# Kernel optimization log

Hardware: AMD Instinct MI355X
Metric: run time of the kernel (lower is better)

The kernel has to match this reference:

```python
import jax, jax.numpy as jnp
import numpy as np

N, E, G = 10000, 40000, 64   # nodes, edges, graphs
ED, H, OUT = 4, 64, 4        # edge_attr_dim, hidden, output_dim


def _nnconv(x, src, dst, edge_attr, w1, b1, w2, b2, root_w, bias, in_dim, out_dim, n_nodes):
    # edge MLP: Linear -> ReLU -> Linear, producing per-edge [in_dim, out_dim] weights
    h = jax.nn.relu(edge_attr @ w1 + b1) @ w2 + b2        # [E, in*out]
    W = h.reshape(-1, in_dim, out_dim)                    # [E, in, out]
    msg = jnp.einsum('ei,eio->eo', x[src], W)             # gather + per-edge matmul
    s = jax.ops.segment_sum(msg, dst, num_segments=n_nodes)
    cnt = jax.ops.segment_sum(jnp.ones((msg.shape[0],), x.dtype), dst, num_segments=n_nodes)
    agg = s / jnp.maximum(cnt, 1.0)[:, None]              # scatter-mean (0 for isolated nodes)
    return agg + x @ root_w + bias                        # NNConv root weight + bias


def setup_inputs():
    key = jax.random.key(0)
    ks = jax.random.split(key, 16)
    lin = lambda k, i, o: jax.random.normal(k, (i, o), jnp.float32) * 0.05
    inp = {}
    inp['node_ids'] = jax.random.normal(ks[0], (N, 1), jnp.float32)
    inp['edge_index'] = jax.random.randint(ks[1], (2, E), 0, N)
    inp['edge_attr'] = jax.random.normal(ks[2], (E, ED), jnp.float32)
    inp['batch'] = jnp.sort(jax.random.randint(ks[3], (N,), 0, G))
    # layer 0: in=1, out=H
    inp['w1_0'] = lin(ks[4], ED, 1 * H); inp['b1_0'] = jnp.zeros((1 * H,), jnp.float32)
    inp['w2_0'] = lin(ks[5], 1 * H, 1 * H); inp['b2_0'] = jnp.zeros((1 * H,), jnp.float32)
    inp['root_0'] = lin(ks[6], 1, H); inp['bias_0'] = jnp.zeros((H,), jnp.float32)
    # layer 1: in=H, out=H
    inp['w1_1'] = lin(ks[7], ED, H * H); inp['b1_1'] = jnp.zeros((H * H,), jnp.float32)
    inp['w2_1'] = lin(ks[8], H * H, H * H); inp['b2_1'] = jnp.zeros((H * H,), jnp.float32)
    inp['root_1'] = lin(ks[9], H, H); inp['bias_1'] = jnp.zeros((H,), jnp.float32)
    # classifier
    inp['wc1'] = lin(ks[10], H, H); inp['bc1'] = jnp.zeros((H,), jnp.float32)
    inp['wc2'] = lin(ks[11], H, OUT); inp['bc2'] = jnp.zeros((OUT,), jnp.float32)
    return inp


def reference(node_ids, edge_index, edge_attr, batch,
              w1_0, b1_0, w2_0, b2_0, root_0, bias_0,
              w1_1, b1_1, w2_1, b2_1, root_1, bias_1,
              wc1, bc1, wc2, bc2):
    src, dst = edge_index[0], edge_index[1]
    x = node_ids
    x = jax.nn.relu(_nnconv(x, src, dst, edge_attr, w1_0, b1_0, w2_0, b2_0, root_0, bias_0, 1, H, N))
    x = jax.nn.relu(_nnconv(x, src, dst, edge_attr, w1_1, b1_1, w2_1, b2_1, root_1, bias_1, H, H, N))
    # dropout omitted (inference mode)
    gs = jax.ops.segment_sum(x, batch, num_segments=G)
    gc = jax.ops.segment_sum(jnp.ones((N,), x.dtype), batch, num_segments=G)
    pooled = gs / jnp.maximum(gc, 1.0)[:, None]           # global_mean_pool
    h = jax.nn.relu(pooled @ wc1 + bc1)
    return h @ wc2 + bc2
```

## Files before the change

kernel.cpp:

```cpp
#include <hip/hip_runtime.h>
#include <hip/hip_fp16.h>

#define N_NODES 10000
#define N_EDGES 40000
#define N_GRAPH 64
#define KKREAL  262144
#define KKTOT   262272
#define BROW    KKTOT
#define EPAD    40192
#define PSLICE  (EPAD * 64)

typedef _Float16 half8_t  __attribute__((ext_vector_type(8)));
typedef float    floatx16 __attribute__((ext_vector_type(16)));

__device__ __forceinline__ void gload_lds16(const void* g, void* l) {
  __builtin_amdgcn_global_load_lds((const __attribute__((address_space(1))) void*)g,
                                   (__attribute__((address_space(3))) void*)l, 16, 0, 0);
}

__device__ __host__ __forceinline__ int swz(int row) {
  return ((row & 3) << 1) | ((row >> 2) & 1);
}

__device__ __forceinline__ half8_t splat8(_Float16 v) {
  half8_t r = {v, v, v, v, v, v, v, v};
  return r;
}

__global__ void prep_B(const float* __restrict__ w2, const float* __restrict__ b2,
                       _Float16* __restrict__ Bws) {
  int kk = blockIdx.x * blockDim.x + threadIdx.x;
  if (kk >= KKTOT) return;
  int s = (kk >> 3) & 15, j3 = kk & 7;
  int basekk = kk & ~127;
  for (int o = 0; o < 64; ++o) {
    int kk_l = basekk | ((s ^ swz(o)) << 3) | j3;
    int k = kk_l >> 6, i = kk_l & 63;
    float v;
    if (k < 4096)       v = w2[k * 4096 + i * 64 + o];
    else if (k == 4096) v = b2[i * 64 + o];
    else                v = 0.f;
    Bws[(size_t)o * BROW + kk] = (_Float16)v;
  }
}

__global__ void layer0_edge(const float* __restrict__ node_ids,
                            const int* __restrict__ ei,
                            const float* __restrict__ ea,
                            const float* __restrict__ w1, const float* __restrict__ b1,
                            const float* __restrict__ w2, const float* __restrict__ b2,
                            float* __restrict__ agg0, float* __restrict__ cnt) {
  __shared__ float w1s[256], b1s[64], w2s[4096], b2s[64], zb[4][64];
  int t = threadIdx.x;
  for (int idx = t; idx < 4096; idx += 256) w2s[idx] = w2[idx];
  if (t < 256) w1s[t] = w1[t];
  if (t < 64) { b1s[t] = b1[t]; b2s[t] = b2[t]; }
  __syncthreads();
  int w = t >> 6, l = t & 63;
  int gw = blockIdx.x * 4 + w;
  int nw = gridDim.x * 4;
  for (int e = gw; e < N_EDGES; e += nw) {
    float a0 = ea[e * 4 + 0], a1 = ea[e * 4 + 1], a2 = ea[e * 4 + 2], a3 = ea[e * 4 + 3];
    float z = a0 * w1s[l] + a1 * w1s[64 + l] + a2 * w1s[128 + l] + a3 * w1s[192 + l] + b1s[l];
    zb[w][l] = fmaxf(z, 0.f);
    asm volatile("s_waitcnt lgkmcnt(0)" ::: "memory");
    __builtin_amdgcn_sched_barrier(0);
    float h = b2s[l];
    #pragma unroll
    for (int k = 0; k < 64; ++k) h += zb[w][k] * w2s[k * 64 + l];
    int src = ei[e], dst = ei[N_EDGES + e];
    float msg = node_ids[src] * h;
    atomicAdd(&agg0[dst * 64 + l], msg);
    if (l == 0) atomicAdd(&cnt[dst], 1.0f);
  }
}

__global__ void node0(const float* __restrict__ node_ids, const int* __restrict__ batch,
                      const float* __restrict__ agg0, const float* __restrict__ cnt,
                      const float* __restrict__ root0, const float* __restrict__ bias0,
                      float* __restrict__ x1, float* __restrict__ pcnt) {
  int gid = blockIdx.x * 256 + threadIdx.x;
  if (gid >= N_NODES * 64) return;
  int n = gid >> 6, o = gid & 63;
  float c = fmaxf(cnt[n], 1.f);
  float v = agg0[gid] / c + node_ids[n] * root0[o] + bias0[o];
  x1[gid] = fmaxf(v, 0.f);
  if (o == 0) atomicAdd(&pcnt[batch[n]], 1.0f);
}

template <bool PART>
__launch_bounds__(256, 3)
__global__ void fused_edge_gemm(const int* __restrict__ ei,
                                const float* __restrict__ ea,
                                const float* __restrict__ x1,
                                const float* __restrict__ w1, const float* __restrict__ b1,
                                const _Float16* __restrict__ Bws,
                                float* __restrict__ outbuf) {
  __shared__ __attribute__((aligned(16))) _Float16 Bl[2][64 * 128];
  __shared__ __attribute__((aligned(16))) __half2 w1q[256][4];
  __shared__ __half2 b1p[256];
  int t = threadIdx.x;
  int ks = blockIdx.x & 7;
  int eb = blockIdx.x >> 3;
  int e0 = eb * 256;
  int w = t >> 6, l = t & 63;
  int half_ = l >> 5;
  int lane31 = l & 31;
  int swo = swz(lane31);

  int kb = ks * 512;
  {
    int j = t;
    #pragma unroll
    for (int d = 0; d < 4; ++d) {
      float2 v = *(const float2*)(w1 + d * 4096 + kb + 2 * j);
      w1q[j][d] = __floats2half2_rn(v.x, v.y);
    }
    float2 bv = *(const float2*)(b1 + kb + 2 * j);
    b1p[j] = __floats2half2_rn(bv.x, bv.y);
  }

  half8_t xh8[2][4];
  __half2 eb_bc[2][4];
  #pragma unroll
  for (int m = 0; m < 2; ++m) {
    int e = e0 + w * 64 + m * 32 + lane31;
    if (e < N_EDGES) {
      int src = ei[e];
      const float* xp = x1 + src * 64 + half_ * 8;
      #pragma unroll
      for (int q = 0; q < 4; ++q) {
        float4 f0 = *(const float4*)(xp + q * 16);
        float4 f1 = *(const float4*)(xp + q * 16 + 4);
        half8_t v;
        v[0] = (_Float16)f0.x; v[1] = (_Float16)f0.y;
        v[2] = (_Float16)f0.z; v[3] = (_Float16)f0.w;
        v[4] = (_Float16)f1.x; v[5] = (_Float16)f1.y;
        v[6] = (_Float16)f1.z; v[7] = (_Float16)f1.w;
        xh8[m][q] = v;
      }
      float4 av = *(const float4*)(ea + e * 4);
      eb_bc[m][0] = __float2half2_rn(av.x); eb_bc[m][1] = __float2half2_rn(av.y);
      eb_bc[m][2] = __float2half2_rn(av.z); eb_bc[m][3] = __float2half2_rn(av.w);
    } else {
      #pragma unroll
      for (int q = 0; q < 4; ++q) xh8[m][q] = splat8((_Float16)0.f);
      #pragma unroll
      for (int d = 0; d < 4; ++d) eb_bc[m][d] = __float2half2_rn(0.f);
    }
  }

  floatx16 acc[2][2];
  #pragma unroll
  for (int m = 0; m < 2; ++m)
    #pragma unroll
    for (int n = 0; n < 2; ++n)
      #pragma unroll
      for (int r = 0; r < 16; ++r) acc[m][n][r] = 0.f;

  int nchunk = (ks == 7) ? 257 : 256;
  size_t sbase_b = (size_t)ks * 65536;
  const char* Bb = (const char*)Bws;

  const char* srcp[4];
  {
    int colb = (l & 15) * 16;
    #pragma unroll
    for (int j = 0; j < 4; ++j) {
      int row = w * 16 + j * 4 + (l >> 4);
      srcp[j] = Bb + sbase_b + (size_t)row * (BROW * 2) + colb;
    }
  }
  char* dst0 = (char*)&Bl[0][0] + w * 4096 + l * 16;
  char* dst1 = (char*)&Bl[1][0] + w * 4096 + l * 16;

  auto stage = [&](int buf) {
    char* dstb = buf ? dst1 : dst0;
    #pragma unroll
    for (int j = 0; j < 4; ++j) {
      gload_lds16(srcp[j], dstb + j * 1024);
      srcp[j] += 256;
    }
  };

  stage(0);
  __syncthreads();

  const __half zero1 = __float2half(0.f);
  union H2F { __half2 h2; _Float16 f[2]; };

  int cur = 0;
  for (int c = 0; c < nchunk; ++c) {
    if (c + 1 < nchunk) stage(cur ^ 1);

    half8_t zs8[2][2];
    if (c < 256) {
      __half2 w0 = w1q[c][0], w1v = w1q[c][1], w2v = w1q[c][2], w3v = w1q[c][3];
      __half2 bv = b1p[c];
      #pragma unroll
      for (int m = 0; m < 2; ++m) {
        __half2 h = __hfma2(eb_bc[m][0], w0, bv);
        h = __hfma2(eb_bc[m][1], w1v, h);
        h = __hfma2(eb_bc[m][2], w2v, h);
        h = __hfma2(eb_bc[m][3], w3v, h);
        H2F u; u.h2 = __halves2half2(__hmax(__low2half(h),  zero1),
                                     __hmax(__high2half(h), zero1));
        zs8[m][0] = splat8(u.f[0]);
        zs8[m][1] = splat8(u.f[1]);
      }
    } else {
      #pragma unroll
      for (int m = 0; m < 2; ++m) {
        zs8[m][0] = splat8((_Float16)1.f);
        zs8[m][1] = splat8((_Float16)0.f);
      }
    }

    const char* blc = (const char*)&Bl[cur][0] + lane31 * 256;
    #pragma unroll
    for (int t8 = 0; t8 < 8; ++t8) {
      int slot = (t8 * 2 + half_) ^ swo;
      const char* ba = blc + slot * 16;
      half8_t bf0 = *(const half8_t*)ba;
      half8_t bf1 = *(const half8_t*)(ba + 8192);
      #pragma unroll
      for (int m = 0; m < 2; ++m) {
        half8_t af = xh8[m][t8 & 3] * zs8[m][t8 >> 2];
        acc[m][0] = __builtin_amdgcn_mfma_f32_32x32x16_f16(af, bf0, acc[m][0], 0, 0, 0);
        acc[m][1] = __builtin_amdgcn_mfma_f32_32x32x16_f16(af, bf1, acc[m][1], 0, 0, 0);
      }
    }

    __syncthreads();
    cur ^= 1;
  }

  if (PART) {
    float* pb = outbuf + ((size_t)ks * EPAD + e0 + w * 64) * 64 + lane31;
    #pragma unroll
    for (int m = 0; m < 2; ++m) {
      #pragma unroll
      for (int r = 0; r < 16; ++r) {
        int row = m * 32 + (r & 3) + 8 * (r >> 2) + 4 * half_;
        pb[(size_t)row * 64]      = acc[m][0][r];
        pb[(size_t)row * 64 + 32] = acc[m][1][r];
      }
    }
  } else {
    #pragma unroll
    for (int m = 0; m < 2; ++m) {
      #pragma unroll
      for (int r = 0; r < 16; ++r) {
        int e = e0 + w * 64 + m * 32 + (r & 3) + 8 * (r >> 2) + 4 * half_;
        if (e < N_EDGES) {
          int dst = ei[N_EDGES + e];
          atomicAdd(&outbuf[dst * 64 + lane31],      acc[m][0][r]);
          atomicAdd(&outbuf[dst * 64 + lane31 + 32], acc[m][1][r]);
        }
      }
    }
  }
}

__global__ void reduce_partials(const float* __restrict__ P8, const int* __restrict__ ei,
                                float* __restrict__ agg1) {
  int gid = blockIdx.x * 256 + threadIdx.x;
  if (gid >= N_EDGES * 64) return;
  int e = gid >> 6;
  float s = 0.f;
  #pragma unroll
  for (int ks = 0; ks < 8; ++ks) s += P8[(size_t)ks * PSLICE + gid];
  int dst = ei[N_EDGES + e];
  atomicAdd(&agg1[dst * 64 + (gid & 63)], s);
}

__global__ void node1_pool(const int* __restrict__ batch, const float* __restrict__ x1,
                           const float* __restrict__ agg1, const float* __restrict__ cnt,
                           const float* __restrict__ root1, const float* __restrict__ bias1,
                           float* __restrict__ psum) {
  __shared__ float rt[4096];
  int t = threadIdx.x;
  for (int idx = t; idx < 4096; idx += 256) rt[idx] = root1[idx];
  __syncthreads();
  int w = t >> 6, l = t & 63;
  int n = blockIdx.x * 4 + w;
  if (n >= N_NODES) return;
  float c = fmaxf(cnt[n], 1.f);
  float acc = agg1[n * 64 + l] / c + bias1[l];
  const float* xp = x1 + n * 64;
  #pragma unroll
  for (int i4 = 0; i4 < 16; ++i4) {
    float4 xv = *(const float4*)(xp + i4 * 4);
    acc += xv.x * rt[(i4 * 4 + 0) * 64 + l] + xv.y * rt[(i4 * 4 + 1) * 64 + l]
         + xv.z * rt[(i4 * 4 + 2) * 64 + l] + xv.w * rt[(i4 * 4 + 3) * 64 + l];
  }
  acc = fmaxf(acc, 0.f);
  atomicAdd(&psum[batch[n] * 64 + l], acc);
}

__global__ void classifier(const float* __restrict__ psum, const float* __restrict__ pcnt,
                           const float* __restrict__ wc1, const float* __restrict__ bc1,
                           const float* __restrict__ wc2, const float* __restrict__ bc2,
                           float* __restrict__ out) {
  __shared__ float hb[64];
  int g = blockIdx.x, j = threadIdx.x;
  float c = fmaxf(pcnt[g], 1.f);
  float h = bc1[j];
  const float* pp = psum + g * 64;
  #pragma unroll
  for (int i4 = 0; i4 < 16; ++i4) {
    float4 pv = *(const float4*)(pp + i4 * 4);
    h += (pv.x / c) * wc1[(i4 * 4 + 0) * 64 + j] + (pv.y / c) * wc1[(i4 * 4 + 1) * 64 + j]
       + (pv.z / c) * wc1[(i4 * 4 + 2) * 64 + j] + (pv.w / c) * wc1[(i4 * 4 + 3) * 64 + j];
  }
  hb[j] = fmaxf(h, 0.f);
  __syncthreads();
  if (j < 4) {
    float o = bc2[j];
    #pragma unroll
    for (int k = 0; k < 64; ++k) o += hb[k] * wc2[k * 4 + j];
    out[g * 4 + j] = o;
  }
}

extern "C" void kernel_launch(void* const* d_in, const int* in_sizes, int n_in,
                              void* d_out, int out_size, void* d_ws, size_t ws_size,
                              hipStream_t stream) {
  const float* node_ids = (const float*)d_in[0];
  const int*   ei       = (const int*)d_in[1];
  const float* ea       = (const float*)d_in[2];
  const int*   batch    = (const int*)d_in[3];
  const float* w1_0 = (const float*)d_in[4];
  const float* b1_0 = (const float*)d_in[5];
  const float* w2_0 = (const float*)d_in[6];
  const float* b2_0 = (const float*)d_in[7];
  const float* root0 = (const float*)d_in[8];
  const float* bias0 = (const float*)d_in[9];
  const float* w1_1 = (const float*)d_in[10];
  const float* b1_1 = (const float*)d_in[11];
  const float* w2_1 = (const float*)d_in[12];
  const float* b2_1 = (const float*)d_in[13];
  const float* root1 = (const float*)d_in[14];
  const float* bias1 = (const float*)d_in[15];
  const float* wc1 = (const float*)d_in[16];
  const float* bc1 = (const float*)d_in[17];
  const float* wc2 = (const float*)d_in[18];
  const float* bc2 = (const float*)d_in[19];
  float* out = (float*)d_out;

  char* ws = (char*)d_ws;
  _Float16* Bws = (_Float16*)ws;
  float* x1   = (float*)(ws + 33570816);
  float* agg0 = (float*)(ws + 36130816);
  float* agg1 = (float*)(ws + 38690816);
  float* cnt  = (float*)(ws + 41250816);
  float* psum = (float*)(ws + 41290816);
  float* pcnt = (float*)(ws + 41307200);
  float* P8   = (float*)(ws + 41307456);
  const size_t NEED_PART = 41307456ull + (size_t)8 * PSLICE * 4;

  (void)hipMemsetAsync(agg0, 0, 2560000 + 2560000 + 40000 + 16384 + 256, stream);

  prep_B<<<(KKTOT + 255) / 256, 256, 0, stream>>>(w2_1, b2_1, Bws);
  layer0_edge<<<512, 256, 0, stream>>>(node_ids, ei, ea, w1_0, b1_0, w2_0, b2_0, agg0, cnt);
  node0<<<(N_NODES * 64 + 255) / 256, 256, 0, stream>>>(node_ids, batch, agg0, cnt, root0, bias0, x1, pcnt);

  if (ws_size >= NEED_PART) {
    fused_edge_gemm<true><<<157 * 8, 256, 0, stream>>>(ei, ea, x1, w1_1, b1_1, Bws, P8);
    reduce_partials<<<(N_EDGES * 64) / 256, 256, 0, stream>>>(P8, ei, agg1);
  } else {
    fused_edge_gemm<false><<<157 * 8, 256, 0, stream>>>(ei, ea, x1, w1_1, b1_1, Bws, agg1);
  }

  node1_pool<<<(N_NODES + 3) / 4, 256, 0, stream>>>(batch, x1, agg1, cnt, root1, bias1, psum);
  classifier<<<N_GRAPH, 64, 0, stream>>>(psum, pcnt, wc1, bc1, wc2, bc2, out);
}
```

Baseline: 1.236 ms.

## Store precomputed B weights chunk-contiguous and raise occupancy of fused edge GEMM

The weight tensor for layer 1 is now laid out so that each 16KB chunk (64 output rows by 128 k values) sits contiguously per k-slice, replacing the row-major layout with a large row stride. Staging into LDS becomes four sequential 1KB loads from a single pointer instead of four strided row pointers. Edge attributes are packed into two half2 registers instead of four broadcast ones, and launch bounds are raised from 3 to 4 blocks per SM to increase occupancy. The costs are a slightly larger workspace, a different prep kernel pattern, and possible register spilling under the tighter bound.

After: 1.473 ms. 19.2% more time.

```diff
diff --git a/kernel.cpp b/kernel.cpp
--- a/kernel.cpp
+++ b/kernel.cpp
@@ -6,7 +6,7 @@
 #define N_GRAPH 64
 #define KKREAL  262144
 #define KKTOT   262272
-#define BROW    KKTOT
+#define CPS     257
 #define EPAD    40192
 #define PSLICE  (EPAD * 64)
 
@@ -28,19 +28,29 @@
 }
 
 __global__ void prep_B(const float* __restrict__ w2, const float* __restrict__ b2,
-                       _Float16* __restrict__ Bws) {
-  int kk = blockIdx.x * blockDim.x + threadIdx.x;
-  if (kk >= KKTOT) return;
-  int s = (kk >> 3) & 15, j3 = kk & 7;
-  int basekk = kk & ~127;
-  for (int o = 0; o < 64; ++o) {
-    int kk_l = basekk | ((s ^ swz(o)) << 3) | j3;
-    int k = kk_l >> 6, i = kk_l & 63;
-    float v;
-    if (k < 4096)       v = w2[k * 4096 + i * 64 + o];
-    else if (k == 4096) v = b2[i * 64 + o];
-    else                v = 0.f;
-    Bws[(size_t)o * BROW + kk] = (_Float16)v;
+                       _Float16* __restrict__ BC) {
+  int tid = blockIdx.x * 256 + threadIdx.x;
+  if (tid >= 8 * CPS * 64) return;
+  int ks  = tid / (CPS * 64);
+  int rem = tid - ks * (CPS * 64);
+  int c = rem >> 6;
+  int o = rem & 63;
+  if (c == 256 && ks != 7) return;
+  _Float16* dst = BC + (size_t)tid * 128;
+  int swo = swz(o);
+  int kkbase = ks * 32768 + c * 128;
+  for (int sp = 0; sp < 16; ++sp) {
+    int kk0 = kkbase + ((sp ^ swo) * 8);
+    #pragma unroll
+    for (int j3 = 0; j3 < 8; ++j3) {
+      int kk_l = kk0 + j3;
+      int k = kk_l >> 6, i = kk_l & 63;
+      float v;
+      if (k < 4096)       v = w2[k * 4096 + i * 64 + o];
+      else if (k == 4096) v = b2[i * 64 + o];
+      else                v = 0.f;
+      dst[sp * 8 + j3] = (_Float16)v;
+    }
   }
 }
 
@@ -89,12 +99,12 @@
 }
 
 template <bool PART>
-__launch_bounds__(256, 3)
+__launch_bounds__(256, 4)
 __global__ void fused_edge_gemm(const int* __restrict__ ei,
                                 const float* __restrict__ ea,
                                 const float* __restrict__ x1,
                                 const float* __restrict__ w1, const float* __restrict__ b1,
-                                const _Float16* __restrict__ Bws,
+                                const _Float16* __restrict__ BC,
                                 float* __restrict__ outbuf) {
   __shared__ __attribute__((aligned(16))) _Float16 Bl[2][64 * 128];
   __shared__ __attribute__((aligned(16))) __half2 w1q[256][4];
@@ -121,7 +131,7 @@
   }
 
   half8_t xh8[2][4];
-  __half2 eb_bc[2][4];
+  __half2 ea01[2], ea23[2];
   #pragma unroll
   for (int m = 0; m < 2; ++m) {
     int e = e0 + w * 64 + m * 32 + lane31;
@@ -140,13 +150,13 @@
         xh8[m][q] = v;
       }
       float4 av = *(const float4*)(ea + e * 4);
-      eb_bc[m][0] = __float2half2_rn(av.x); eb_bc[m][1] = __float2half2_rn(av.y);
-      eb_bc[m][2] = __float2half2_rn(av.z); eb_bc[m][3] = __float2half2_rn(av.w);
+      ea01[m] = __floats2half2_rn(av.x, av.y);
+      ea23[m] = __floats2half2_rn(av.z, av.w);
     } else {
       #pragma unroll
       for (int q = 0; q < 4; ++q) xh8[m][q] = splat8((_Float16)0.f);
-      #pragma unroll
-      for (int d = 0; d < 4; ++d) eb_bc[m][d] = __float2half2_rn(0.f);
+      ea01[m] = __float2half2_rn(0.f);
+      ea23[m] = __float2half2_rn(0.f);
     }
   }
 
@@ -159,31 +169,20 @@
       for (int r = 0; r < 16; ++r) acc[m][n][r] = 0.f;
 
   int nchunk = (ks == 7) ? 257 : 256;
-  size_t sbase_b = (size_t)ks * 65536;
-  const char* Bb = (const char*)Bws;
-
-  const char* srcp[4];
-  {
-    int colb = (l & 15) * 16;
-    #pragma unroll
-    for (int j = 0; j < 4; ++j) {
-      int row = w * 16 + j * 4 + (l >> 4);
-      srcp[j] = Bb + sbase_b + (size_t)row * (BROW * 2) + colb;
-    }
-  }
+
+  const char* gp = (const char*)BC + (size_t)ks * (CPS * 16384) + w * 4096 + l * 16;
   char* dst0 = (char*)&Bl[0][0] + w * 4096 + l * 16;
   char* dst1 = (char*)&Bl[1][0] + w * 4096 + l * 16;
 
-  auto stage = [&](int buf) {
-    char* dstb = buf ? dst1 : dst0;
-    #pragma unroll
-    for (int j = 0; j < 4; ++j) {
-      gload_lds16(srcp[j], dstb + j * 1024);
-      srcp[j] += 256;
-    }
+  auto stage = [&](char* dstb) {
+    gload_lds16(gp,        dstb);
+    gload_lds16(gp + 1024, dstb + 1024);
+    gload_lds16(gp + 2048, dstb + 2048);
+    gload_lds16(gp + 3072, dstb + 3072);
+    gp += 16384;
   };
 
-  stage(0);
+  stage(dst0);
   __syncthreads();
 
   const __half zero1 = __float2half(0.f);
@@ -191,7 +190,7 @@
 
   int cur = 0;
   for (int c = 0; c < nchunk; ++c) {
-    if (c + 1 < nchunk) stage(cur ^ 1);
+    if (c + 1 < nchunk) stage(cur ? dst0 : dst1);
 
     half8_t zs8[2][2];
     if (c < 256) {
@@ -199,10 +198,10 @@
       __half2 bv = b1p[c];
       #pragma unroll
       for (int m = 0; m < 2; ++m) {
-        __half2 h = __hfma2(eb_bc[m][0], w0, bv);
-        h = __hfma2(eb_bc[m][1], w1v, h);
-        h = __hfma2(eb_bc[m][2], w2v, h);
-        h = __hfma2(eb_bc[m][3], w3v, h);
+        __half2 h = __hfma2(__half2half2(__low2half(ea01[m])),  w0,  bv);
+        h = __hfma2(__half2half2(__high2half(ea01[m])), w1v, h);
+        h = __hfma2(__half2half2(__low2half(ea23[m])),  w2v, h);
+        h = __hfma2(__half2half2(__high2half(ea23[m])), w3v, h);
         H2F u; u.h2 = __halves2half2(__hmax(__low2half(h),  zero1),
                                      __hmax(__high2half(h), zero1));
         zs8[m][0] = splat8(u.f[0]);
@@ -349,27 +348,27 @@
   float* out = (float*)d_out;
 
   char* ws = (char*)d_ws;
-  _Float16* Bws = (_Float16*)ws;
-  float* x1   = (float*)(ws + 33570816);
-  float* agg0 = (float*)(ws + 36130816);
-  float* agg1 = (float*)(ws + 38690816);
-  float* cnt  = (float*)(ws + 41250816);
-  float* psum = (float*)(ws + 41290816);
-  float* pcnt = (float*)(ws + 41307200);
-  float* P8   = (float*)(ws + 41307456);
-  const size_t NEED_PART = 41307456ull + (size_t)8 * PSLICE * 4;
+  _Float16* BC = (_Float16*)ws;
+  float* x1   = (float*)(ws + 33685504);
+  float* agg0 = (float*)(ws + 36245504);
+  float* agg1 = (float*)(ws + 38805504);
+  float* cnt  = (float*)(ws + 41365504);
+  float* psum = (float*)(ws + 41405504);
+  float* pcnt = (float*)(ws + 41421888);
+  float* P8   = (float*)(ws + 41422144);
+  const size_t NEED_PART = 41422144ull + (size_t)8 * PSLICE * 4;
 
   (void)hipMemsetAsync(agg0, 0, 2560000 + 2560000 + 40000 + 16384 + 256, stream);
 
-  prep_B<<<(KKTOT + 255) / 256, 256, 0, stream>>>(w2_1, b2_1, Bws);
+  prep_B<<<(8 * CPS * 64 + 255) / 256, 256, 0, stream>>>(w2_1, b2_1, BC);
   layer0_edge<<<512, 256, 0, stream>>>(node_ids, ei, ea, w1_0, b1_0, w2_0, b2_0, agg0, cnt);
   node0<<<(N_NODES * 64 + 255) / 256, 256, 0, stream>>>(node_ids, batch, agg0, cnt, root0, bias0, x1, pcnt);
 
   if (ws_size >= NEED_PART) {
-    fused_edge_gemm<true><<<157 * 8, 256, 0, stream>>>(ei, ea, x1, w1_1, b1_1, Bws, P8);
+    fused_edge_gemm<true><<<157 * 8, 256, 0, stream>>>(ei, ea, x1, w1_1, b1_1, BC, P8);
     reduce_partials<<<(N_EDGES * 64) / 256, 256, 0, stream>>>(P8, ei, agg1);
   } else {
-    fused_edge_gemm<false><<<157 * 8, 256, 0, stream>>>(ei, ea, x1, w1_1, b1_1, Bws, agg1);
+    fused_edge_gemm<false><<<157 * 8, 256, 0, stream>>>(ei, ea, x1, w1_1, b1_1, BC, agg1);
   }
 
   node1_pool<<<(N_NODES + 3) / 4, 256, 0, stream>>>(batch, x1, agg1, cnt, root1, bias1, psum);
```
